# Performance work log

Hardware: AMD Instinct MI355X
Metric: run time of the kernel (lower is better)

The kernel has to match this reference:

```python
import jax, jax.numpy as jnp
import numpy as np
import math
from jax import lax

L_SIDE = 16  # l, so sequence length L = l*l = 256


def _compute_kernel(A1, A2, A3, A4, B1, B2, C1, C2, l):
    """Builds the (l^2, l^2, D) impulse-response kernel of the coupled 2D SSM.

    Faithful to TwoDimensionalSSM.compute_x_matrix/_compute_kernel:
      x_h[i,j] = a1*x_h[i,j-1] + a2*x_v[i,j-1];  x_h[i,j, i*l+j] = b1
      x_v[i,j] = a3*x_h[i-1,j] + a4*x_v[i-1,j];  x_v[i,j, i*l+j] = b2
      kernel   = einsum('pqdn,hn->pqh', x_h, C1) + einsum('pqdn,hn->pqh', x_v, C2)
    (note: the original einsum sums over the state's embed dim D as well).
    """
    sig = lambda t: jax.nn.sigmoid(t) * 0.5
    a1, a2, a3, a4, b1, b2 = sig(A1), sig(A2), sig(A3), sig(A4), sig(B1), sig(B2)
    D, N = a1.shape
    L2 = l * l
    js = jnp.arange(l)
    z_col = jnp.zeros((L2, D, N), a1.dtype)

    def inner(carry, xs):
        # scan over columns j within a row: x_h[i,j] depends on (i, j-1)
        xh_prev, xv_prev = carry          # (L2, D, N)
        xv_j, ch = xs                     # xv_j: (L2, D, N), ch: scalar channel i*l+j
        xh_j = a1 * xh_prev + a2 * xv_prev
        xh_j = xh_j.at[ch].set(b1)
        return (xh_j, xv_j), xh_j

    def outer(carry, i):
        # scan over rows i: x_v[i] depends elementwise on row i-1
        xh_row, xv_row = carry            # (l, L2, D, N)
        xv_new = a3 * xh_row + a4 * xv_row
        chans = i * l + js                # (l,)
        xv_new = xv_new.at[js, chans].set(b2)
        _, xh_new = lax.scan(inner, (z_col, z_col), (xv_new, chans))
        return (xh_new, xv_new), (xh_new, xv_new)

    z_row = jnp.zeros((l, L2, D, N), a1.dtype)
    _, (x_h, x_v) = lax.scan(outer, (z_row, z_row), jnp.arange(l))
    x_h = x_h.reshape(L2, L2, D, N)
    x_v = x_v.reshape(L2, L2, D, N)
    kernel = jnp.einsum('pqdn,hn->pqh', x_h, C1) + jnp.einsum('pqdn,hn->pqh', x_v, C2)
    return kernel  # (L2, L2, D)


def setup_inputs() -> dict:
    key = jax.random.key(0)
    ks = jax.random.split(key, 10)
    D, N = 256, 2
    L, B = L_SIDE * L_SIDE, 32
    p = lambda k, shape, std: jax.random.normal(k, shape, dtype=jnp.float32) * std
    return {
        'x': p(ks[0], (L, B, D), 1.0),
        'A1': p(ks[1], (D, N), 0.2),
        'A2': p(ks[2], (D, N), 0.2),
        'A3': p(ks[3], (D, N), 0.2),
        'A4': p(ks[4], (D, N), 0.2),
        'B1': p(ks[5], (D, N), 0.2),
        'B2': p(ks[6], (D, N), 0.2),
        'C1': p(ks[7], (D, N), 1.0),
        'C2': p(ks[8], (D, N), 1.0),
        'omega': p(ks[9], (D,), 1.0),
    }


def reference(x, A1, A2, A3, A4, B1, B2, C1, C2, omega):
    L, B, D = x.shape
    l = int(math.isqrt(L))
    residual = x * omega                       # (L, B, D)
    xt = jnp.transpose(x, (1, 2, 0))           # (B, D, L)
    k = _compute_kernel(A1, A2, A3, A4, B1, B2, C1, C2, l)  # (L, L, D)
    # apply full impulse-response matrix of the 2D SSM (exact, no truncation)
    out = jnp.einsum('pqd,bdq->bdp', k, xt)    # (B, D, L)
    out = jnp.transpose(out, (2, 0, 1))        # (L, B, D)
    return jax.nn.silu(out + residual)
```

## Files before the change

kernel.cpp:

```cpp
#include <hip/hip_runtime.h>
#include <hip/hip_bf16.h>
#include <math.h>


#define NPROD 16

__device__ __forceinline__ float sigh(float t) { return 0.5f / (1.0f + __expf(-t)); }

__global__ __launch_bounds__(256) void ssm_one(
    const float* __restrict__ x,
    const float* __restrict__ A1, const float* __restrict__ A2,
    const float* __restrict__ A3, const float* __restrict__ A4,
    const float* __restrict__ B1, const float* __restrict__ B2,
    const float* __restrict__ C1, const float* __restrict__ C2,
    const float* __restrict__ omega,
    float* __restrict__ out, float* __restrict__ P,
    volatile float* __restrict__ guard)
{
    __shared__ float xs[256 * 32];
    __shared__ float gsum[1024];
    __shared__ float ks[32][260];
    __shared__ float buf[2][32][36];
    int bx = blockIdx.x;
    int t  = threadIdx.x;

    if (bx < NPROD) {
        int dl = t & 15, nn = (t >> 4) & 1;
        int idx = (bx * 16 + dl) * 2 + nn;
        float a1 = sigh(A1[idx]), a2 = sigh(A2[idx]);
        float a3 = sigh(A3[idx]), a4 = sigh(A4[idx]);
        float b1 = sigh(B1[idx]), b2 = sigh(B2[idx]);
        float gh[16], gv[16], acc16[16];
        #pragma unroll
        for (int j = 0; j < 16; ++j) gv[j] = 0.f;
        gv[0] = b2;
        gh[0] = b1;
        #pragma unroll
        for (int j = 1; j < 16; ++j) gh[j] = a1 * gh[j-1] + a2 * gv[j-1];
        int vL = t & 31, nR = t >> 5;
        for (int di = 0; di < 16; ++di) {
            int pb = di & 1;
            if (t < 32) {
                float4* wp = (float4*)&buf[pb][t][0];
                wp[0] = make_float4(gh[0],  gh[1],  gh[2],  gh[3]);
                wp[1] = make_float4(gh[4],  gh[5],  gh[6],  gh[7]);
                wp[2] = make_float4(gh[8],  gh[9],  gh[10], gh[11]);
                wp[3] = make_float4(gh[12], gh[13], gh[14], gh[15]);
                wp[4] = make_float4(gv[0],  gv[1],  gv[2],  gv[3]);
                wp[5] = make_float4(gv[4],  gv[5],  gv[6],  gv[7]);
                wp[6] = make_float4(gv[8],  gv[9],  gv[10], gv[11]);
                wp[7] = make_float4(gv[12], gv[13], gv[14], gv[15]);
            }
            __syncthreads();
            float v[16];
            if (t < 64) {
                #pragma unroll
                for (int i = 0; i < 16; ++i) v[i] = buf[pb][nR * 16 + i][vL];
            }
            float ghn[16], gvn[16];
            if (di < 15) {
                #pragma unroll
                for (int j = 0; j < 16; ++j) gvn[j] = a3 * gh[j] + a4 * gv[j];
                ghn[0] = 0.f;
                #pragma unroll
                for (int j = 1; j < 16; ++j) ghn[j] = a1 * ghn[j-1] + a2 * gvn[j-1];
            }
            if (t < 64) {
                #pragma unroll
                for (int st = 8; st >= 1; st >>= 1)
                    #pragma unroll
                    for (int i = 0; i < st; ++i) v[i] += v[i + st];
                acc16[di] = v[0];
            }
            if (di < 15) {
                #pragma unroll
                for (int j = 0; j < 16; ++j) { gh[j] = ghn[j]; gv[j] = gvn[j]; }
            }
        }
        if (t < 64) {
            int type = vL >> 4, j = vL & 15;
            int base = (bx * 4 + nR * 2 + type) * 256 + j;
            #pragma unroll
            for (int di = 0; di < 16; ++di) P[base + di * 16] = acc16[di];
        }
        __threadfence();
        __syncthreads();
        if (t == 0) guard[bx] = 1.0f;
        return;
    }

    int cb = bx - NPROD;
    int b  = cb >> 3;
    int h0 = (cb & 7) * 32;
    #pragma unroll
    for (int it = 0; it < 32; ++it) {
        int idx = it * 256 + t;
        int q = idx >> 5, hl = idx & 31;
        __builtin_amdgcn_global_load_lds(
            (const __attribute__((address_space(1))) void*)(x + (size_t)q * 8192 + b * 256 + h0 + hl),
            (__attribute__((address_space(3))) void*)(&xs[idx]), 4, 0, 0);
    }
    if (t == 0) {
        bool ok = false;
        while (!ok) {
            ok = true;
            #pragma unroll
            for (int g = 0; g < NPROD; ++g)
                if (guard[g] != 1.0f) ok = false;
            if (!ok) __builtin_amdgcn_s_sleep(2);
        }
    }
    __syncthreads();
    {
        int o = t * 4;
        int pn = o >> 9, pt = (o >> 8) & 1, pc = o & 255;
        const float4* P4 = (const float4*)P;
        float4 a = make_float4(0.f, 0.f, 0.f, 0.f);
        #pragma unroll
        for (int g = 0; g < 16; ++g) {
            float4 v = P4[(g * 4 + pn * 2 + pt) * 64 + (pc >> 2)];
            a.x += v.x; a.y += v.y; a.z += v.z; a.w += v.w;
        }
        *(float4*)&gsum[o] = a;
    }
    __syncthreads();
    int hl = t & 31;
    int slot = t >> 5;
    int h = h0 + hl;
    float c10 = C1[2*h], c11 = C1[2*h+1], c20 = C2[2*h], c21 = C2[2*h+1];
    float om = omega[h];
    #pragma unroll
    for (int cg2 = 0; cg2 < 8; ++cg2) {
        int cell = slot * 32 + cg2 * 4;
        float4 gh0 = *(const float4*)&gsum[cell];
        float4 gv0 = *(const float4*)&gsum[256 + cell];
        float4 gh1 = *(const float4*)&gsum[512 + cell];
        float4 gv1 = *(const float4*)&gsum[768 + cell];
        float4 r;
        r.x = c10 * gh0.x + c11 * gh1.x + c20 * gv0.x + c21 * gv1.x;
        r.y = c10 * gh0.y + c11 * gh1.y + c20 * gv0.y + c21 * gv1.y;
        r.z = c10 * gh0.z + c11 * gh1.z + c20 * gv0.z + c21 * gv1.z;
        r.w = c10 * gh0.w + c11 * gh1.w + c20 * gv0.w + c21 * gv1.w;
        *(float4*)&ks[hl][cell] = r;
    }
    __syncthreads();
    int rslot = slot;
    #pragma unroll
    for (int rr = 0; rr < 2; ++rr) {
        int i = rr ? (15 - rslot) : rslot;
        float acc[16];
        #pragma unroll
        for (int j = 0; j < 16; ++j) acc[j] = 0.f;
        for (int di = 0; di <= i; ++di) {
            int srow = i - di;
            float4 k0 = *(const float4*)&ks[hl][di * 16];
            float4 k1 = *(const float4*)&ks[hl][di * 16 + 4];
            float4 k2 = *(const float4*)&ks[hl][di * 16 + 8];
            float4 k3v = *(const float4*)&ks[hl][di * 16 + 12];
            float kr[16] = {k0.x, k0.y, k0.z, k0.w, k1.x, k1.y, k1.z, k1.w,
                            k2.x, k2.y, k2.z, k2.w, k3v.x, k3v.y, k3v.z, k3v.w};
            #pragma unroll
            for (int s = 0; s < 16; ++s) {
                float xv = xs[(srow * 16 + s) * 32 + hl];
                #pragma unroll
                for (int u = 0; u + s < 16; ++u) acc[s+u] += kr[u] * xv;
            }
        }
        #pragma unroll
        for (int j = 0; j < 16; ++j) {
            int p = i * 16 + j;
            float vv = acc[j] + xs[p * 32 + hl] * om;
            out[(size_t)p * 8192 + b * 256 + h0 + hl] = vv / (1.f + __expf(-vv));
        }
    }
}

extern "C" void kernel_launch(void* const* d_in, const int* in_sizes, int n_in,
                              void* d_out, int out_size, void* d_ws, size_t ws_size,
                              hipStream_t stream) {
    const float* x  = (const float*)d_in[0];
    const float* A1 = (const float*)d_in[1];
    const float* A2 = (const float*)d_in[2];
    const float* A3 = (const float*)d_in[3];
    const float* A4 = (const float*)d_in[4];
    const float* B1 = (const float*)d_in[5];
    const float* B2 = (const float*)d_in[6];
    const float* C1 = (const float*)d_in[7];
    const float* C2 = (const float*)d_in[8];
    const float* omega = (const float*)d_in[9];
    float* out = (float*)d_out;
    float* P   = (float*)d_ws;
    volatile float* guard = (volatile float*)(P + NPROD * 1024);
    hipLaunchKernelGGL(ssm_one, dim3(NPROD + 256), dim3(256), 0, stream,
                       x, A1, A2, A3, A4, B1, B2, C1, C2, omega, out, P, guard);
}
```

Measured before the change: 19.01 us.

## Centralize producer reduction in block 0 and transpose x tile for vector LDS reads

Producer block 0 now waits for the other producers, reduces their partial sums into a single GHGV buffer, and signals a second guard. The 256 consumer blocks then copy 1024 floats instead of each reducing 16 partials. The x tile in LDS is stored transposed with padded rows (channel-major, stride 260), so the inner convolution loop and the residual can use float4 loads instead of 16 scalar loads. This adds a serial reduction step on block 0 before any consumer can proceed, and the global-to-LDS load becomes uncoalesced, with extra padding loads.

```diff
diff --git a/kernel.cpp b/kernel.cpp
--- a/kernel.cpp
+++ b/kernel.cpp
@@ -14,10 +14,10 @@
     const float* __restrict__ B1, const float* __restrict__ B2,
     const float* __restrict__ C1, const float* __restrict__ C2,
     const float* __restrict__ omega,
-    float* __restrict__ out, float* __restrict__ P,
+    float* __restrict__ out, float* __restrict__ P, float* __restrict__ GHGV,
     volatile float* __restrict__ guard)
 {
-    __shared__ float xs[256 * 32];
+    __shared__ float xs2[32 * 260];
     __shared__ float gsum[1024];
     __shared__ float ks[32][260];
     __shared__ float buf[2][32][36];
@@ -86,43 +86,60 @@
         __threadfence();
         __syncthreads();
         if (t == 0) guard[bx] = 1.0f;
+        if (bx == 0) {
+            if (t == 0) {
+                bool ok = false;
+                while (!ok) {
+                    ok = true;
+                    #pragma unroll
+                    for (int g = 1; g < NPROD; ++g)
+                        if (guard[g] != 1.0f) ok = false;
+                    if (!ok) __builtin_amdgcn_s_sleep(2);
+                }
+            }
+            __syncthreads();
+            __threadfence();
+            int o = t * 4;
+            int pn = o >> 9, pt = (o >> 8) & 1, pc = o & 255;
+            const float4* P4 = (const float4*)P;
+            float4 a = make_float4(0.f, 0.f, 0.f, 0.f);
+            #pragma unroll
+            for (int g = 0; g < 16; ++g) {
+                float4 v = P4[(g * 4 + pn * 2 + pt) * 64 + (pc >> 2)];
+                a.x += v.x; a.y += v.y; a.z += v.z; a.w += v.w;
+            }
+            *(float4*)&GHGV[o] = a;
+            __threadfence();
+            __syncthreads();
+            if (t == 0) guard[NPROD] = 1.0f;
+        }
         return;
     }
 
     int cb = bx - NPROD;
     int b  = cb >> 3;
     int h0 = (cb & 7) * 32;
-    #pragma unroll
-    for (int it = 0; it < 32; ++it) {
-        int idx = it * 256 + t;
-        int q = idx >> 5, hl = idx & 31;
-        __builtin_amdgcn_global_load_lds(
-            (const __attribute__((address_space(1))) void*)(x + (size_t)q * 8192 + b * 256 + h0 + hl),
-            (__attribute__((address_space(3))) void*)(&xs[idx]), 4, 0, 0);
+    {
+        const size_t xoff = (size_t)b * 256 + h0;
+        #pragma unroll
+        for (int it = 0; it < 33; ++it) {
+            int idx = it * 256 + t;
+            if (idx < 32 * 260) {
+                int hl2 = idx / 260;
+                int q   = idx - hl2 * 260;
+                int qq  = (q < 256) ? q : 0;
+                __builtin_amdgcn_global_load_lds(
+                    (const __attribute__((address_space(1))) void*)(x + (size_t)qq * 8192 + xoff + hl2),
+                    (__attribute__((address_space(3))) void*)(&xs2[idx]), 4, 0, 0);
+            }
+        }
     }
     if (t == 0) {
-        bool ok = false;
-        while (!ok) {
-            ok = true;
-            #pragma unroll
-            for (int g = 0; g < NPROD; ++g)
-                if (guard[g] != 1.0f) ok = false;
-            if (!ok) __builtin_amdgcn_s_sleep(2);
-        }
+        while (guard[NPROD] != 1.0f) __builtin_amdgcn_s_sleep(2);
     }
     __syncthreads();
-    {
-        int o = t * 4;
-        int pn = o >> 9, pt = (o >> 8) & 1, pc = o & 255;
-        const float4* P4 = (const float4*)P;
-        float4 a = make_float4(0.f, 0.f, 0.f, 0.f);
-        #pragma unroll
-        for (int g = 0; g < 16; ++g) {
-            float4 v = P4[(g * 4 + pn * 2 + pt) * 64 + (pc >> 2)];
-            a.x += v.x; a.y += v.y; a.z += v.z; a.w += v.w;
-        }
-        *(float4*)&gsum[o] = a;
-    }
+    __threadfence();
+    *(float4*)&gsum[t * 4] = *(const float4*)&GHGV[t * 4];
     __syncthreads();
     int hl = t & 31;
     int slot = t >> 5;
@@ -159,17 +176,29 @@
             float4 k3v = *(const float4*)&ks[hl][di * 16 + 12];
             float kr[16] = {k0.x, k0.y, k0.z, k0.w, k1.x, k1.y, k1.z, k1.w,
                             k2.x, k2.y, k2.z, k2.w, k3v.x, k3v.y, k3v.z, k3v.w};
+            const float* xrow = &xs2[hl * 260 + srow * 16];
+            float4 x0 = *(const float4*)&xrow[0];
+            float4 x1 = *(const float4*)&xrow[4];
+            float4 x2 = *(const float4*)&xrow[8];
+            float4 x3 = *(const float4*)&xrow[12];
+            float xr[16] = {x0.x, x0.y, x0.z, x0.w, x1.x, x1.y, x1.z, x1.w,
+                            x2.x, x2.y, x2.z, x2.w, x3.x, x3.y, x3.z, x3.w};
             #pragma unroll
-            for (int s = 0; s < 16; ++s) {
-                float xv = xs[(srow * 16 + s) * 32 + hl];
-                #pragma unroll
-                for (int u = 0; u + s < 16; ++u) acc[s+u] += kr[u] * xv;
-            }
-        }
+            for (int s = 0; s < 16; ++s)
+                #pragma unroll
+                for (int u = 0; u + s < 16; ++u) acc[s+u] += kr[u] * xr[s];
+        }
+        const float* xpr = &xs2[hl * 260 + i * 16];
+        float4 r0 = *(const float4*)&xpr[0];
+        float4 r1 = *(const float4*)&xpr[4];
+        float4 r2 = *(const float4*)&xpr[8];
+        float4 r3 = *(const float4*)&xpr[12];
+        float xres[16] = {r0.x, r0.y, r0.z, r0.w, r1.x, r1.y, r1.z, r1.w,
+                          r2.x, r2.y, r2.z, r2.w, r3.x, r3.y, r3.z, r3.w};
         #pragma unroll
         for (int j = 0; j < 16; ++j) {
             int p = i * 16 + j;
-            float vv = acc[j] + xs[p * 32 + hl] * om;
+            float vv = acc[j] + xres[j] * om;
             out[(size_t)p * 8192 + b * 256 + h0 + hl] = vv / (1.f + __expf(-vv));
         }
     }
@@ -188,9 +217,11 @@
     const float* C1 = (const float*)d_in[7];
     const float* C2 = (const float*)d_in[8];
     const float* omega = (const float*)d_in[9];
-    float* out = (float*)d_out;
-    float* P   = (float*)d_ws;
-    volatile float* guard = (volatile float*)(P + NPROD * 1024);
+    float* out  = (float*)d_out;
+    float* P    = (float*)d_ws;
+    float* GHGV = P + NPROD * 1024;
+    volatile float* guard = (volatile float*)(GHGV + 1024);
     hipLaunchKernelGGL(ssm_one, dim3(NPROD + 256), dim3(256), 0, stream,
-                       x, A1, A2, A3, A4, B1, B2, C1, C2, omega, out, P, guard);
+                       x, A1, A2, A3, A4, B1, B2, C1, C2, omega, out, P, GHGV,
+                       (volatile float*)guard);
 }
```

After: 37.83 us. +99.0%, slower.
